# Performance work log

Hardware: AMD Instinct MI355X
Metric: run time of the kernel (lower is better)

The kernel has to match this reference:

```python
import jax, jax.numpy as jnp
import numpy as np

B, T, D_MODEL, HEAD_DIM = 4, 4096, 1024, 64

def setup_inputs() -> dict:
    key = jax.random.key(0)
    ks = jax.random.split(key, 7)
    s = 1.0 / np.sqrt(D_MODEL)
    return {
        "x": jax.random.normal(ks[0], (B, T, D_MODEL), dtype=jnp.float32),
        "Wq": jax.random.uniform(ks[1], (D_MODEL, HEAD_DIM), jnp.float32, -s, s),
        "bq": jax.random.uniform(ks[2], (HEAD_DIM,), jnp.float32, -s, s),
        "Wk": jax.random.uniform(ks[3], (D_MODEL, HEAD_DIM), jnp.float32, -s, s),
        "bk": jax.random.uniform(ks[4], (HEAD_DIM,), jnp.float32, -s, s),
        "Wv": jax.random.uniform(ks[5], (D_MODEL, HEAD_DIM), jnp.float32, -s, s),
        "bv": jax.random.uniform(ks[6], (HEAD_DIM,), jnp.float32, -s, s),
    }

def reference(x, Wq, bq, Wk, bk, Wv, bv):
    # x: [B,T,D]; projections -> [B,T,H]
    q = jnp.einsum("btd,dh->bth", x, Wq) + bq
    k = jnp.einsum("btd,dh->bth", x, Wk) + bk
    v = jnp.einsum("btd,dh->bth", x, Wv) + bv
    scale = HEAD_DIM ** -0.5
    # scores: [B,Tq,Tk] -- naive full attention matrix (memory-bound)
    scores = jnp.einsum("bqh,bkh->bqk", q, k) * scale
    neg = jnp.finfo(scores.dtype).min
    T_ = scores.shape[-1]
    causal = jnp.triu(jnp.full((T_, T_), neg, dtype=scores.dtype), k=1)
    scores = scores + causal[None, :, :]
    probs = jax.nn.softmax(scores, axis=-1)
    y = jnp.einsum("bqk,bkh->bqh", probs, v)
    return y
```

## Files before the change

kernel.cpp:

```cpp
#include <hip/hip_runtime.h>
#include <hip/hip_bf16.h>

typedef __attribute__((ext_vector_type(4))) float f4v;
typedef __attribute__((ext_vector_type(16))) float f16v;
typedef __attribute__((ext_vector_type(4))) unsigned short u16x4;
typedef __attribute__((ext_vector_type(8))) unsigned short u16x8;
typedef __attribute__((ext_vector_type(4))) unsigned int u32x4;
typedef __attribute__((ext_vector_type(8))) __bf16 bf16x8;
typedef __attribute__((ext_vector_type(8))) _Float16 h8v;

#define D_MODEL 1024
#define HDIM 64
#define TSEQ 4096
#define QB 32
#define QSCALE 0.18033688011112042f

__device__ __forceinline__ unsigned short f2bf(float f) {
    union { float f; unsigned u; } v; v.f = f;
    unsigned r = v.u + 0x7FFFu + ((v.u >> 16) & 1u);
    return (unsigned short)(r >> 16);
}
__device__ __forceinline__ bf16x8 ld8(const unsigned short* p) {
    return __builtin_bit_cast(bf16x8, *(const u16x8*)p);
}
__device__ __forceinline__ h8v ldh8(const unsigned short* p) {
    return __builtin_bit_cast(h8v, *(const u16x8*)p);
}
__device__ __forceinline__ f4v mfma16f(h8v a, h8v b, f4v c) {
    return __builtin_amdgcn_mfma_f32_16x16x32_f16(a, b, c, 0, 0, 0);
}
__device__ __forceinline__ f16v mfma32(bf16x8 a, bf16x8 b, f16v c) {
    return __builtin_amdgcn_mfma_f32_32x32x16_bf16(a, b, c, 0, 0, 0);
}
__device__ __forceinline__ unsigned cvtpk(float a, float b) {
    unsigned r;
    asm("v_cvt_pk_bf16_f32 %0, %1, %2" : "=v"(r) : "v"(a), "v"(b));
    return r;
}
__device__ __forceinline__ void pswap(unsigned& a, unsigned& b) {
    asm("v_permlane32_swap_b32 %0, %1" : "+v"(a), "+v"(b));
}
__device__ __forceinline__ h8v pack8(f4v a, f4v b) {
    unsigned p0 = __builtin_bit_cast(unsigned, __builtin_amdgcn_cvt_pkrtz(a[0], a[1]));
    unsigned p1 = __builtin_bit_cast(unsigned, __builtin_amdgcn_cvt_pkrtz(a[2], a[3]));
    unsigned p2 = __builtin_bit_cast(unsigned, __builtin_amdgcn_cvt_pkrtz(b[0], b[1]));
    unsigned p3 = __builtin_bit_cast(unsigned, __builtin_amdgcn_cvt_pkrtz(b[2], b[3]));
    u32x4 u = {p0, p1, p2, p3};
    return __builtin_bit_cast(h8v, u);
}

__global__ void prep_wf(const float* __restrict__ Wq, const float* __restrict__ Wk,
                        const float* __restrict__ Wv, unsigned short* __restrict__ Wf)
{
    int idx = blockIdx.x * 256 + threadIdx.x;
    int j = idx & 7, lane = (idx >> 3) & 63, nf = (idx >> 9) & 3,
        kstep = (idx >> 11) & 31, m = idx >> 16;
    int k = kstep * 32 + 8 * (lane >> 4) + j;
    int n = nf * 16 + (lane & 15);
    const float* W = (m == 0) ? Wq : (m == 1) ? Wk : Wv;
    _Float16 hv = (_Float16)W[k * 64 + n];
    Wf[idx] = __builtin_bit_cast(unsigned short, hv);
}

__global__ __launch_bounds__(256, 2)
void proj_qkv(const float* __restrict__ x, const unsigned short* __restrict__ Wf,
              const float* __restrict__ bq, const float* __restrict__ bk,
              const float* __restrict__ bv,
              unsigned short* __restrict__ Qf, unsigned short* __restrict__ Kf,
              unsigned short* __restrict__ Vf)
{
    __shared__ float xs[2][2048];
    __shared__ unsigned short wl[2][12288];

    const int tid = threadIdx.x;
    const int w = tid >> 6, l = tid & 63;
    const int row0 = blockIdx.x * 32;

    f4v acc[2][3];
#pragma unroll
    for (int s = 0; s < 2; ++s)
#pragma unroll
        for (int f = 0; f < 3; ++f) acc[s][f] = (f4v)0.f;

    auto stage = [&](int buf, int t) {
#pragma unroll
        for (int j = 0; j < 2; ++j) {
            const int G = j * 256 + tid;
            const int row = G >> 4;
            const int gl = (G & 15) ^ (row & 7);
            const float* src = x + (size_t)(row0 + row) * D_MODEL + t * 64 + gl * 4;
            __builtin_amdgcn_global_load_lds(
                (const __attribute__((address_space(1))) unsigned*)src,
                (__attribute__((address_space(3))) unsigned*)&xs[buf][G * 4],
                16, 0, 0);
        }
#pragma unroll
        for (int j = 0; j < 6; ++j) {
            const int chunk = j * 4 + w;
            const int cf = chunk >> 1, ks = chunk & 1;
            const unsigned short* src =
                Wf + ((((cf >> 2) * 32 + (t * 2 + ks)) * 4 + (cf & 3)) << 9) + l * 8;
            __builtin_amdgcn_global_load_lds(
                (const __attribute__((address_space(1))) unsigned*)src,
                (__attribute__((address_space(3))) unsigned*)&wl[buf][chunk * 512],
                16, 0, 0);
        }
    };

    stage(0, 0);
    __syncthreads();

#pragma unroll
    for (int t = 0; t < 16; ++t) {
        if (t < 15) stage((t + 1) & 1, t + 1);
        const int b = t & 1;
        const int sw = l & 7;
#pragma unroll
        for (int ks = 0; ks < 2; ++ks) {
            h8v bw[3];
#pragma unroll
            for (int f = 0; f < 3; ++f) {
                const int cf = w * 3 + f;
                bw[f] = ldh8(&wl[b][(cf * 2 + ks) * 512 + l * 8]);
            }
            const int gr = ks * 8 + 2 * (l >> 4);
#pragma unroll
            for (int s = 0; s < 2; ++s) {
                const int row = s * 16 + (l & 15);
                f4v a0 = *(const f4v*)&xs[b][row * 64 + ((gr ^ sw) << 2)];
                f4v a1 = *(const f4v*)&xs[b][row * 64 + (((gr + 1) ^ sw) << 2)];
                h8v xa = pack8(a0, a1);
#pragma unroll
                for (int f = 0; f < 3; ++f)
                    acc[s][f] = mfma16f(xa, bw[f], acc[s][f]);
            }
        }
        __syncthreads();
    }

    const float* bias[3] = {bq, bk, bv};
#pragma unroll
    for (int s = 0; s < 2; ++s) {
        const int rowb = row0 + s * 16 + 4 * (l >> 4);
        const int b = rowb >> 12, tok0 = rowb & 4095;
#pragma unroll
        for (int f = 0; f < 3; ++f) {
            const int cf = w * 3 + f;
            const int m = cf >> 2, nf = cf & 3;
            const int d = nf * 16 + (l & 15);
            const float bb = bias[m][d];
            if (m == 0) {
                const int qtile = tok0 >> 5;
                const int ksq = d >> 4, hq = (d >> 3) & 1, jq = d & 7;
#pragma unroll
                for (int r4 = 0; r4 < 4; ++r4) {
                    int cq = (tok0 & 31) + r4;
                    Qf[(((size_t)(b * 128 + qtile) * 4 + ksq) << 9) + (32 * hq + cq) * 8 + jq] =
                        f2bf((acc[s][f][r4] + bb) * QSCALE);
                }
            } else if (m == 1) {
                const int t = tok0 >> 6, tb = (tok0 >> 5) & 1;
                const int ksk = d >> 4, hk = (d >> 3) & 1, jk = d & 7;
#pragma unroll
                for (int r4 = 0; r4 < 4; ++r4) {
                    int ck = (tok0 & 31) + r4;
                    Kf[(((size_t)((b * 64 + t) * 8 + tb * 4 + ksk)) << 9) + (32 * hk + ck) * 8 + jk] =
                        f2bf(acc[s][f][r4] + bb);
                }
            } else {
                const int t = tok0 >> 6, ku = (tok0 >> 4) & 3, hv = (tok0 >> 3) & 1, jv = tok0 & 7;
                const int cv = d & 31, td = d >> 5;
                u16x4 pk;
#pragma unroll
                for (int r4 = 0; r4 < 4; ++r4) pk[r4] = f2bf(acc[s][f][r4] + bb);
                *(u16x4*)(Vf + (((size_t)((b * 64 + t) * 8 + td * 4 + ku)) << 9) +
                          (32 * hv + cv) * 8 + jv) = pk;
            }
        }
    }
}

__global__ __launch_bounds__(512, 4)
void attn(const unsigned short* __restrict__ Qf, const unsigned short* __restrict__ Kf,
          const unsigned short* __restrict__ Vf, float* __restrict__ Yg)
{
    __shared__ float Osm[8][QB][33];
    __shared__ float Msm[8][QB];
    __shared__ float Lsm[8][QB];

    const int tid = threadIdx.x;
    const int g8 = tid >> 6, l = tid & 63, h = l >> 5, c = l & 31;
    const int batch = blockIdx.x & 3;
    const int qt = 127 - (blockIdx.x >> 2);
    const int NT = qt + 1;

    bf16x8 qf[4];
    const unsigned short* qp = Qf + (((size_t)(batch * 128 + qt) * 4) << 9) + l * 8;
#pragma unroll
    for (int ks = 0; ks < 4; ++ks) qf[ks] = ld8(qp + (ks << 9));

    float mrun = -1e30f, lrun = 0.f;
    f16v o0 = (f16v)0.f, o1 = (f16v)0.f;

    for (int t = g8; t < NT; t += 8) {
        const size_t kbase = ((size_t)(batch * 64 + (t >> 1)) * 8) << 9;
        const int half = t & 1;
        bf16x8 kr[4];
#pragma unroll
        for (int ks = 0; ks < 4; ++ks)
            kr[ks] = ld8(Kf + kbase + ((size_t)(half * 4 + ks) << 9) + l * 8);
        bf16x8 vr[2][2];
#pragma unroll
        for (int td = 0; td < 2; ++td)
#pragma unroll
            for (int kk = 0; kk < 2; ++kk)
                vr[td][kk] = ld8(Vf + kbase + ((size_t)(td * 4 + 2 * half + kk) << 9) + l * 8);

        f16v sacc = (f16v)0.f;
        __builtin_amdgcn_s_setprio(1);
#pragma unroll
        for (int ks = 0; ks < 4; ++ks) sacc = mfma32(kr[ks], qf[ks], sacc);
        __builtin_amdgcn_s_setprio(0);

        if (t == NT - 1) {
#pragma unroll
            for (int r = 0; r < 16; ++r) {
                int mv = (r & 3) + 8 * (r >> 2) + 4 * h;
                if (mv > c) sacc[r] = -1e30f;
            }
        }
        float pm = -1e30f;
#pragma unroll
        for (int r = 0; r < 16; ++r) pm = fmaxf(pm, sacc[r]);
        pm = fmaxf(pm, __shfl_xor(pm, 32));
        const float mnew = fmaxf(mrun, pm);
        const float sc = exp2f(mrun - mnew);
        mrun = mnew;
        float rs = 0.f;
#pragma unroll
        for (int r = 0; r < 16; ++r) {
            float e = exp2f(sacc[r] - mnew);
            sacc[r] = e; rs += e;
        }
        rs += __shfl_xor(rs, 32);
        lrun = lrun * sc + rs;
#pragma unroll
        for (int r = 0; r < 16; ++r) { o0[r] *= sc; o1[r] *= sc; }
        unsigned wp[8];
#pragma unroll
        for (int i = 0; i < 8; ++i) wp[i] = cvtpk(sacc[2 * i], sacc[2 * i + 1]);
        pswap(wp[0], wp[2]); pswap(wp[1], wp[3]);
        pswap(wp[4], wp[6]); pswap(wp[5], wp[7]);
        u32x4 f0 = {wp[0], wp[1], wp[2], wp[3]};
        u32x4 f1 = {wp[4], wp[5], wp[6], wp[7]};
        bf16x8 pa0 = __builtin_bit_cast(bf16x8, f0);
        bf16x8 pa1 = __builtin_bit_cast(bf16x8, f1);
        __builtin_amdgcn_s_setprio(1);
        o0 = mfma32(vr[0][0], pa0, o0);
        o0 = mfma32(vr[0][1], pa1, o0);
        o1 = mfma32(vr[1][0], pa0, o1);
        o1 = mfma32(vr[1][1], pa1, o1);
        __builtin_amdgcn_s_setprio(0);
    }

    if (h == 0) { Msm[g8][c] = mrun; Lsm[g8][c] = lrun; }

    auto write_partial = [&](const f16v& o) {
#pragma unroll
        for (int r = 0; r < 16; ++r) {
            int dd = (r & 3) + 8 * (r >> 2) + 4 * h;
            Osm[g8][c][dd] = o[r];
        }
    };
    auto merge_phase = [&](int dhalf) {
        const int q = tid >> 4, d2 = (tid & 15) * 2;
        float mm = -1e30f;
#pragma unroll
        for (int gg = 0; gg < 8; ++gg) mm = fmaxf(mm, Msm[gg][q]);
        float L = 0.f, oo0 = 0.f, oo1 = 0.f;
#pragma unroll
        for (int gg = 0; gg < 8; ++gg) {
            float a = exp2f(Msm[gg][q] - mm);
            L += a * Lsm[gg][q];
            oo0 += a * Osm[gg][q][d2];
            oo1 += a * Osm[gg][q][d2 + 1];
        }
        float inv = 1.f / L;
        float* yp = Yg + ((size_t)batch * TSEQ + (size_t)qt * QB + q) * HDIM + dhalf * 32 + d2;
        yp[0] = oo0 * inv; yp[1] = oo1 * inv;
    };

    write_partial(o0);
    __syncthreads();
    merge_phase(0);
    __syncthreads();
    write_partial(o1);
    __syncthreads();
    merge_phase(1);
}

extern "C" void kernel_launch(void* const* d_in, const int* in_sizes, int n_in,
                              void* d_out, int out_size, void* d_ws, size_t ws_size,
                              hipStream_t stream)
{
    const float* x  = (const float*)d_in[0];
    const float* Wq = (const float*)d_in[1];
    const float* bq = (const float*)d_in[2];
    const float* Wk = (const float*)d_in[3];
    const float* bk = (const float*)d_in[4];
    const float* Wv = (const float*)d_in[5];
    const float* bv = (const float*)d_in[6];
    float* y = (float*)d_out;

    unsigned short* Qb = (unsigned short*)d_ws;
    unsigned short* Kb = Qb + (size_t)1048576;
    unsigned short* Vb = Kb + (size_t)1048576;
    unsigned short* Wf = Vb + (size_t)1048576;

    prep_wf<<<768, 256, 0, stream>>>(Wq, Wk, Wv, Wf);
    proj_qkv<<<512, 256, 0, stream>>>(x, Wf, bq, bk, bv, Qb, Kb, Vb);
    attn<<<512, 512, 0, stream>>>(Qb, Kb, Vb, y);
}
```

Baseline: 53.99 us.

## Share K/V tiles across two query blocks via double-buffered LDS staging

The attention kernel now handles 64 queries per block, split into two 32-query halves, so each K/V tile is read from global memory once and reused by both halves. K/V tiles go into a double-buffered 64KB shared-memory region through global_load_lds, so the next tile loads while the current one is computed. Eight waves split the work by query half and key sub-tile, and the causal mask is applied per sub-tile. The intended gain is less global and L2 traffic per query. In exchange there are fewer blocks, lower occupancy (launch bounds 2), a block-wide barrier every iteration, and idle waves on tiles the causal mask skips.

After: 77.96 us. +44.4%, slower.

```diff
diff --git a/kernel.cpp b/kernel.cpp
--- a/kernel.cpp
+++ b/kernel.cpp
@@ -180,114 +180,143 @@
     }
 }
 
-__global__ __launch_bounds__(512, 4)
+__global__ __launch_bounds__(512, 2)
 void attn(const unsigned short* __restrict__ Qf, const unsigned short* __restrict__ Kf,
           const unsigned short* __restrict__ Vf, float* __restrict__ Yg)
 {
-    __shared__ float Osm[8][QB][33];
-    __shared__ float Msm[8][QB];
-    __shared__ float Lsm[8][QB];
+    __shared__ __align__(16) char smem[65536];
+    unsigned short* kvs = (unsigned short*)smem;
+    __shared__ float Msm[8][32];
+    __shared__ float Lsm[8][32];
 
     const int tid = threadIdx.x;
-    const int g8 = tid >> 6, l = tid & 63, h = l >> 5, c = l & 31;
+    const int w8 = tid >> 6, l = tid & 63, h = l >> 5, c = l & 31;
+    const int s = w8 >> 2, t01 = (w8 >> 1) & 1, kh = w8 & 1;
     const int batch = blockIdx.x & 3;
-    const int qt = 127 - (blockIdx.x >> 2);
-    const int NT = qt + 1;
+    const int qsb = 63 - (blockIdx.x >> 2);
+    const int iters = (qsb + 2) >> 1;
+    const int qb = 64 * qsb + 32 * s;
 
     bf16x8 qf[4];
-    const unsigned short* qp = Qf + (((size_t)(batch * 128 + qt) * 4) << 9) + l * 8;
+    const unsigned short* qp = Qf + (((size_t)(batch * 128 + 2 * qsb + s) * 4) << 9) + l * 8;
 #pragma unroll
     for (int ks = 0; ks < 4; ++ks) qf[ks] = ld8(qp + (ks << 9));
 
     float mrun = -1e30f, lrun = 0.f;
     f16v o0 = (f16v)0.f, o1 = (f16v)0.f;
 
-    for (int t = g8; t < NT; t += 8) {
-        const size_t kbase = ((size_t)(batch * 64 + (t >> 1)) * 8) << 9;
-        const int half = t & 1;
-        bf16x8 kr[4];
-#pragma unroll
-        for (int ks = 0; ks < 4; ++ks)
-            kr[ks] = ld8(Kf + kbase + ((size_t)(half * 4 + ks) << 9) + l * 8);
-        bf16x8 vr[2][2];
-#pragma unroll
-        for (int td = 0; td < 2; ++td)
-#pragma unroll
-            for (int kk = 0; kk < 2; ++kk)
-                vr[td][kk] = ld8(Vf + kbase + ((size_t)(td * 4 + 2 * half + kk) << 9) + l * 8);
-
-        f16v sacc = (f16v)0.f;
-        __builtin_amdgcn_s_setprio(1);
-#pragma unroll
-        for (int ks = 0; ks < 4; ++ks) sacc = mfma32(kr[ks], qf[ks], sacc);
-        __builtin_amdgcn_s_setprio(0);
-
-        if (t == NT - 1) {
+    auto stage = [&](int buf, int i) {
+#pragma unroll
+        for (int r = 0; r < 4; ++r) {
+            const int kt = 2 * i + (r >> 1);
+            const unsigned short* src =
+                ((r & 1) ? Vf : Kf) + (((size_t)(batch * 64 + kt) * 8) << 9) + tid * 8;
+            __builtin_amdgcn_global_load_lds(
+                (const __attribute__((address_space(1))) unsigned*)src,
+                (__attribute__((address_space(3))) unsigned*)
+                    (kvs + ((size_t)buf * 16384 + (r * 512 + tid) * 8)),
+                16, 0, 0);
+        }
+    };
+
+    stage(0, 0);
+    __syncthreads();
+
+    for (int i = 0; i < iters; ++i) {
+        const int buf = i & 1;
+        if (i + 1 < iters) stage(buf ^ 1, i + 1);
+        const int kvb = 128 * i + 64 * t01 + 32 * kh;
+        if (kvb <= qb + 31) {
+            unsigned short* kb = kvs + (size_t)buf * 16384 + t01 * 1024 * 8;
+            bf16x8 kr[4], vr[2][2];
+#pragma unroll
+            for (int ks = 0; ks < 4; ++ks)
+                kr[ks] = ld8(kb + ((kh * 4 + ks) * 64 + l) * 8);
+#pragma unroll
+            for (int td = 0; td < 2; ++td)
+#pragma unroll
+                for (int kk = 0; kk < 2; ++kk)
+                    vr[td][kk] = ld8(kb + (512 + (td * 4 + 2 * kh + kk) * 64 + l) * 8);
+
+            f16v sacc = (f16v)0.f;
+            __builtin_amdgcn_s_setprio(1);
+#pragma unroll
+            for (int ks = 0; ks < 4; ++ks) sacc = mfma32(kr[ks], qf[ks], sacc);
+            __builtin_amdgcn_s_setprio(0);
+
+            if (kvb + 31 > qb) {
+#pragma unroll
+                for (int r = 0; r < 16; ++r) {
+                    int mv = (r & 3) + 8 * (r >> 2) + 4 * h;
+                    if (kvb + mv > qb + c) sacc[r] = -1e30f;
+                }
+            }
+            float pm = -1e30f;
+#pragma unroll
+            for (int r = 0; r < 16; ++r) pm = fmaxf(pm, sacc[r]);
+            pm = fmaxf(pm, __shfl_xor(pm, 32));
+            const float mnew = fmaxf(mrun, pm);
+            const float sc = exp2f(mrun - mnew);
+            mrun = mnew;
+            float rs = 0.f;
 #pragma unroll
             for (int r = 0; r < 16; ++r) {
-                int mv = (r & 3) + 8 * (r >> 2) + 4 * h;
-                if (mv > c) sacc[r] = -1e30f;
-            }
-        }
-        float pm = -1e30f;
-#pragma unroll
-        for (int r = 0; r < 16; ++r) pm = fmaxf(pm, sacc[r]);
-        pm = fmaxf(pm, __shfl_xor(pm, 32));
-        const float mnew = fmaxf(mrun, pm);
-        const float sc = exp2f(mrun - mnew);
-        mrun = mnew;
-        float rs = 0.f;
-#pragma unroll
-        for (int r = 0; r < 16; ++r) {
-            float e = exp2f(sacc[r] - mnew);
-            sacc[r] = e; rs += e;
-        }
-        rs += __shfl_xor(rs, 32);
-        lrun = lrun * sc + rs;
-#pragma unroll
-        for (int r = 0; r < 16; ++r) { o0[r] *= sc; o1[r] *= sc; }
-        unsigned wp[8];
-#pragma unroll
-        for (int i = 0; i < 8; ++i) wp[i] = cvtpk(sacc[2 * i], sacc[2 * i + 1]);
-        pswap(wp[0], wp[2]); pswap(wp[1], wp[3]);
-        pswap(wp[4], wp[6]); pswap(wp[5], wp[7]);
-        u32x4 f0 = {wp[0], wp[1], wp[2], wp[3]};
-        u32x4 f1 = {wp[4], wp[5], wp[6], wp[7]};
-        bf16x8 pa0 = __builtin_bit_cast(bf16x8, f0);
-        bf16x8 pa1 = __builtin_bit_cast(bf16x8, f1);
-        __builtin_amdgcn_s_setprio(1);
-        o0 = mfma32(vr[0][0], pa0, o0);
-        o0 = mfma32(vr[0][1], pa1, o0);
-        o1 = mfma32(vr[1][0], pa0, o1);
-        o1 = mfma32(vr[1][1], pa1, o1);
-        __builtin_amdgcn_s_setprio(0);
+                float e = exp2f(sacc[r] - mnew);
+                sacc[r] = e; rs += e;
+            }
+            rs += __shfl_xor(rs, 32);
+            lrun = lrun * sc + rs;
+#pragma unroll
+            for (int r = 0; r < 16; ++r) { o0[r] *= sc; o1[r] *= sc; }
+            unsigned wp[8];
+#pragma unroll
+            for (int ii = 0; ii < 8; ++ii) wp[ii] = cvtpk(sacc[2 * ii], sacc[2 * ii + 1]);
+            pswap(wp[0], wp[2]); pswap(wp[1], wp[3]);
+            pswap(wp[4], wp[6]); pswap(wp[5], wp[7]);
+            u32x4 f0 = {wp[0], wp[1], wp[2], wp[3]};
+            u32x4 f1 = {wp[4], wp[5], wp[6], wp[7]};
+            bf16x8 pa0 = __builtin_bit_cast(bf16x8, f0);
+            bf16x8 pa1 = __builtin_bit_cast(bf16x8, f1);
+            __builtin_amdgcn_s_setprio(1);
+            o0 = mfma32(vr[0][0], pa0, o0);
+            o0 = mfma32(vr[0][1], pa1, o0);
+            o1 = mfma32(vr[1][0], pa0, o1);
+            o1 = mfma32(vr[1][1], pa1, o1);
+            __builtin_amdgcn_s_setprio(0);
+        }
+        __syncthreads();
     }
 
-    if (h == 0) { Msm[g8][c] = mrun; Lsm[g8][c] = lrun; }
+    float (*Osm)[32][33] = (float(*)[32][33])smem;
+    if (h == 0) { Msm[w8][c] = mrun; Lsm[w8][c] = lrun; }
 
     auto write_partial = [&](const f16v& o) {
 #pragma unroll
         for (int r = 0; r < 16; ++r) {
             int dd = (r & 3) + 8 * (r >> 2) + 4 * h;
-            Osm[g8][c][dd] = o[r];
+            Osm[w8][c][dd] = o[r];
         }
     };
     auto merge_phase = [&](int dhalf) {
-        const int q = tid >> 4, d2 = (tid & 15) * 2;
+        const int q6 = tid >> 3, d4 = (tid & 7) * 4;
+        const int st = q6 >> 5, qq = q6 & 31;
         float mm = -1e30f;
 #pragma unroll
-        for (int gg = 0; gg < 8; ++gg) mm = fmaxf(mm, Msm[gg][q]);
-        float L = 0.f, oo0 = 0.f, oo1 = 0.f;
-#pragma unroll
-        for (int gg = 0; gg < 8; ++gg) {
-            float a = exp2f(Msm[gg][q] - mm);
-            L += a * Lsm[gg][q];
-            oo0 += a * Osm[gg][q][d2];
-            oo1 += a * Osm[gg][q][d2 + 1];
+        for (int j = 0; j < 4; ++j) mm = fmaxf(mm, Msm[st * 4 + j][qq]);
+        float L = 0.f;
+        f4v ov = (f4v)0.f;
+#pragma unroll
+        for (int j = 0; j < 4; ++j) {
+            const int gg = st * 4 + j;
+            float a = exp2f(Msm[gg][qq] - mm);
+            L += a * Lsm[gg][qq];
+#pragma unroll
+            for (int e = 0; e < 4; ++e) ov[e] += a * Osm[gg][qq][d4 + e];
         }
         float inv = 1.f / L;
-        float* yp = Yg + ((size_t)batch * TSEQ + (size_t)qt * QB + q) * HDIM + dhalf * 32 + d2;
-        yp[0] = oo0 * inv; yp[1] = oo1 * inv;
+        float* yp = Yg + ((size_t)batch * TSEQ + (size_t)64 * qsb + q6) * HDIM + dhalf * 32 + d4;
+#pragma unroll
+        for (int e = 0; e < 4; ++e) yp[e] = ov[e] * inv;
     };
 
     write_partial(o0);
@@ -319,5 +348,5 @@
 
     prep_wf<<<768, 256, 0, stream>>>(Wq, Wk, Wv, Wf);
     proj_qkv<<<512, 256, 0, stream>>>(x, Wf, bq, bk, bv, Qb, Kb, Vb);
-    attn<<<512, 512, 0, stream>>>(Qb, Kb, Vb, y);
-}
+    attn<<<256, 512, 0, stream>>>(Qb, Kb, Vb, y);
+}
```
